# Optimization experiments

Measured on AMD Instinct MI355X. Metric: run time of the kernel, lower is better.

## Reference

```python
import jax, jax.numpy as jnp
import numpy as np

N, IN_DIM, HID, OUT, NH = 512, 256, 256, 256, 4
HD = OUT // NH  # head_dim = 64
EPS = 1e-5


def _mlp(x, w1, b1, w2, b2):
    return jax.nn.relu(x @ w1 + b1) @ w2 + b2


def setup_inputs() -> dict:
    key = jax.random.key(0)
    ks = jax.random.split(key, 32)

    def rn(k, shape, fan_in):
        return (jax.random.normal(k, shape, jnp.float32) / np.float32(np.sqrt(fan_in)))

    V = jax.random.normal(ks[0], (N, IN_DIM), jnp.float32)
    adj = jax.random.randint(ks[1], (N, N), 0, 2, jnp.int32)
    adj = adj.at[jnp.arange(N), jnp.arange(N)].set(1)  # self-edges: avoid all -inf rows
    prev_hidden = jax.random.normal(ks[2], (N, HID), jnp.float32)
    z = jnp.zeros
    return dict(
        V=V, adj=adj, prev_hidden=prev_hidden,
        W1=rn(ks[3], (IN_DIM, HID), IN_DIM),
        a_std0=rn(ks[4], (HID, 1), HID), a_std1=rn(ks[5], (HID, 1), HID),
        ce_w1=rn(ks[6], (2 * IN_DIM, HID), 2 * IN_DIM), ce_b1=z((HID,), jnp.float32),
        ce_w2=rn(ks[7], (HID, HD), HID), ce_b2=z((HD,), jnp.float32),
        a_c0=rn(ks[8], (HD, 1), HD), a_c1=rn(ks[9], (HD, 1), HD),
        te_w1=rn(ks[10], (IN_DIM + HID, HID), IN_DIM + HID), te_b1=z((HID,), jnp.float32),
        te_w2=rn(ks[11], (HID, HD), HID), te_b2=z((HD,), jnp.float32),
        a_t0=rn(ks[12], (HD, 1), HD), a_t1=rn(ks[13], (HD, 1), HD),
        co_w1=rn(ks[14], (3 * IN_DIM, HID), 3 * IN_DIM), co_b1=z((HID,), jnp.float32),
        co_w2=rn(ks[15], (HID, HD), HID), co_b2=z((HD,), jnp.float32),
        a_co0=rn(ks[16], (HD, 1), HD), a_co1=rn(ks[17], (HD, 1), HD),
        W2=rn(ks[18], (HID + 2 * HD + 1, OUT), HID + 2 * HD + 1),
        Wo=rn(ks[19], (OUT, OUT), OUT), bo=z((OUT,), jnp.float32),
        ln_g=jnp.ones((OUT,), jnp.float32), ln_b=z((OUT,), jnp.float32),
    )


def reference(V, adj, prev_hidden, W1, a_std0, a_std1,
              ce_w1, ce_b1, ce_w2, ce_b2, a_c0, a_c1,
              te_w1, te_b1, te_w2, te_b2, a_t0, a_t1,
              co_w1, co_b1, co_w2, co_b2, a_co0, a_co1,
              W2, Wo, bo, ln_g, ln_b):
    ninf = -jnp.inf

    # ---- standard GAT branch -> H1: (N, HID) ----
    Wh1 = V @ W1
    s1 = Wh1 @ a_std0 + (Wh1 @ a_std1).T                      # (N, N)
    s1 = jnp.where(adj == 0, ninf, s1)
    H1 = jax.nn.softmax(s1, axis=1) @ Wh1

    # ---- causal branch: all ordered pairs i!=j, global softmax -> H2: (N, HD) ----
    pair = jnp.concatenate([jnp.broadcast_to(V[:, None, :], (N, N, IN_DIM)),
                            jnp.broadcast_to(V[None, :, :], (N, N, IN_DIM))], axis=-1)
    cf = _mlp(pair, ce_w1, ce_b1, ce_w2, ce_b2)               # (N, N, HD)
    cs = (cf @ (a_c0 + a_c1))[..., 0]                         # (N, N)
    cs = jnp.where(jnp.eye(N, dtype=bool), ninf, cs)          # exclude i==j pairs
    ca = jax.nn.softmax(cs.reshape(-1)).reshape(N, N, 1)
    H2 = jnp.broadcast_to((ca * cf).sum((0, 1)), (N, HD))

    # ---- temporal branch: (N,1) scores broadcast against causal mask -> running mean ----
    tf = _mlp(jnp.concatenate([V, prev_hidden], axis=-1), te_w1, te_b1, te_w2, te_b2)  # (N, HD)
    ts = tf @ (a_t0 + a_t1)                                   # (N, 1)
    cmask = jnp.triu(jnp.ones((N, N), bool), 1)
    tsb = jnp.where(cmask, ninf, jnp.broadcast_to(ts, (N, N)))
    H3 = jax.nn.softmax(tsb, axis=1) @ tf                     # (N, HD)

    # ---- coop branch: first two neighbors by index; size-1 softmax; buggy pad -> (N,1) ----
    order = jnp.argsort((1 - adj).astype(jnp.int32), axis=1, stable=True)  # adj==1 first, index order
    nb = V[order[:, :2]]                                      # (N, 2, IN_DIM)
    valid = ((adj == 1).sum(axis=1) >= 2)
    nb = jnp.where(valid[:, None, None], nb, jnp.zeros_like(nb))
    ci = jnp.concatenate([V, nb[:, 0], nb[:, 1]], axis=-1)    # (N, 3*IN_DIM)
    cf4 = _mlp(ci, co_w1, co_b1, co_w2, co_b2)                # (N, HD)
    ca4 = jax.nn.softmax(cf4 @ (a_co0 + a_co1), axis=1)       # (N,1): softmax over size-1 -> ones
    h4vec = (ca4.T @ cf4)[0]                                  # (HD,)
    # original: squeeze(-2)->(HD,), dim==1 -> unsqueeze(-1)->(HD,1), zero-pad rows to N
    H4 = jnp.zeros((N, 1), V.dtype).at[:HD, 0].set(h4vec)

    # ---- combine, lazy W2, proj, LN, ELU (dropout identity in eval) ----
    Hc = jnp.concatenate([H1, H2, H3, H4], axis=-1) @ W2      # (N, OUT)
    out = Hc @ Wo + bo
    mu = out.mean(-1, keepdims=True)
    var = ((out - mu) ** 2).mean(-1, keepdims=True)
    out = (out - mu) / jnp.sqrt(var + EPS) * ln_g + ln_b
    return jax.nn.elu(out)
```

## Files before the change

### kernel.cpp

```cpp
#include <hip/hip_runtime.h>
#include <math.h>

#define NN 512
#define HD 64
#define EPSV 1e-5f

typedef unsigned short u16;
typedef short s4v __attribute__((ext_vector_type(4)));
typedef short s8v __attribute__((ext_vector_type(8)));
typedef float f4v __attribute__((ext_vector_type(4)));

struct GD {
  const float *A, *A2, *A3, *A4;
  const int* I;
  const float *B, *bias;
  float* C;
  const u16 *Bth, *Btl;
  u16 *Cth, *Ctl;
  int Bkp, Ckp;
  int M, K, Nn, mode, act;
};

#define GEMM_SMEM 28800
#define MEGA_SMEM 38656

__device__ __forceinline__ void split_bf16(float x, u16& h, u16& l) {
  unsigned xb = __float_as_uint(x);
  float hf = __uint_as_float(xb & 0xffff0000u);
  h = (u16)(xb >> 16);
  l = (u16)(__float_as_uint(x - hf) >> 16);
}

__device__ __forceinline__ void gemm_body(char* smem, const GD& d, int bx, int by) {
  u16 (*Ah)[72] = (u16(*)[72])smem;
  u16 (*Al)[72] = (u16(*)[72])(smem + 4608);
  u16 (*Bh)[68] = (u16(*)[68])(smem + 9216);
  u16 (*Bl)[68] = (u16(*)[68])(smem + 9216 + 8704);
  char* extra = smem + 26624;
  int* nbl = (int*)extra;
  float* wscl = (float*)extra;
  float* rowsuml = wscl + 512;

  const int t = threadIdx.x;
  const int rowbase = by * 32, colbase = bx * 64;
  const int K = d.K, Nn = d.Nn, mode = d.mode, M = d.M;
  if (rowbase >= M) return;

  if (mode == 2) {
    int wave = t >> 6, lane = t & 63;
    for (int rr = wave; rr < 32; rr += 4) {
      int row = rowbase + rr;
      int n0 = -1, n1 = -1, cnt = 0;
      for (int c = 0; c < 8; ++c) {
        unsigned long long mm = __ballot(d.I[row * NN + c * 64 + lane] != 0);
        cnt += (int)__popcll(mm);
        if (n0 < 0 && mm) { n0 = c * 64 + (int)__builtin_ctzll(mm); mm &= mm - 1; }
        if (n1 < 0 && mm) { n1 = c * 64 + (int)__builtin_ctzll(mm); }
      }
      if (lane == 0) { nbl[rr * 3] = n0; nbl[rr * 3 + 1] = n1; nbl[rr * 3 + 2] = (cnt >= 2); }
    }
    __syncthreads();
  } else if (mode == 4) {
    wscl[t] = d.A2[t];
    wscl[256 + t] = d.A2[256 + t];
    __syncthreads();
  }

  float4 aR[2], bR[4];
  s8v bp[4];
  float rs0 = 0.f, rs1 = 0.f;

  auto loadA = [&](int k0) {
#pragma unroll
    for (int j = 0; j < 2; ++j) {
      int idx = t + j * 256;
      int r = idx >> 4, c0 = (idx & 15) * 4;
      int row = rowbase + r, gk = k0 + c0;
      float4 v4 = make_float4(0.f, 0.f, 0.f, 0.f);
      if (mode == 0) {
        if (row < M && gk < K) v4 = *(const float4*)&d.A[(size_t)row * K + gk];
      } else if (mode == 1) {
        if (gk < 256) v4 = *(const float4*)&d.A[row * 256 + gk];
        else v4 = *(const float4*)&d.A2[row * 256 + gk - 256];
      } else if (mode == 2) {
        int seg = gk >> 8;
        int src = (seg == 0) ? row : (nbl[r * 3 + 2] ? nbl[r * 3 + seg - 1] : -1);
        if (src >= 0) v4 = *(const float4*)&d.A[src * 256 + (gk & 255)];
      } else if (mode == 3) {
        if (gk + 3 < 256) v4 = *(const float4*)&d.A[row * 256 + gk];
        else if (gk >= 256 && gk + 3 < 320) v4 = *(const float4*)&d.A2[gk - 256];
        else if (gk >= 320 && gk + 3 < 384) v4 = *(const float4*)&d.A3[row * 64 + gk - 320];
        else if (gk == 384) v4.x = (row < 64) ? d.A4[row] : 0.f;
      } else {
        int4 a4 = *(const int4*)&d.I[row * NN + gk];
        v4.x = a4.x ? wscl[gk + 0] : 0.f;
        v4.y = a4.y ? wscl[gk + 1] : 0.f;
        v4.z = a4.z ? wscl[gk + 2] : 0.f;
        v4.w = a4.w ? wscl[gk + 3] : 0.f;
        float ss = v4.x + v4.y + v4.z + v4.w;
        if (j == 0) rs0 += ss; else rs1 += ss;
      }
      aR[j] = v4;
    }
  };
  auto loadB = [&](int k0) {
    if (d.Bth) {
#pragma unroll
      for (int j = 0; j < 2; ++j) {
        int idx = t + j * 256;
        int n = idx >> 3, kb = (idx & 7) * 8;
        size_t base = (size_t)(colbase + n) * d.Bkp + k0 + kb;
        bp[j] = *(const s8v*)&d.Bth[base];
        bp[2 + j] = *(const s8v*)&d.Btl[base];
      }
    } else {
#pragma unroll
      for (int j = 0; j < 4; ++j) {
        int idx = t + j * 256;
        int r = idx >> 4, c0 = (idx & 15) * 4;
        int gk = k0 + r;
        float4 v4 = make_float4(0.f, 0.f, 0.f, 0.f);
        if (gk < K) v4 = *(const float4*)&d.B[(size_t)gk * Nn + colbase + c0];
        bR[j] = v4;
      }
    }
  };
  auto stos = [&]() {
#pragma unroll
    for (int j = 0; j < 2; ++j) {
      int idx = t + j * 256;
      int r = idx >> 4, c0 = (idx & 15) * 4;
      float v[4] = {aR[j].x, aR[j].y, aR[j].z, aR[j].w};
      u16 h[4], l[4];
#pragma unroll
      for (int e = 0; e < 4; ++e) split_bf16(v[e], h[e], l[e]);
      *(short4*)&Ah[r][c0] = make_short4((short)h[0], (short)h[1], (short)h[2], (short)h[3]);
      *(short4*)&Al[r][c0] = make_short4((short)l[0], (short)l[1], (short)l[2], (short)l[3]);
    }
    if (d.Bth) {
#pragma unroll
      for (int j = 0; j < 2; ++j) {
        int idx = t + j * 256;
        int n = idx >> 3, kb = (idx & 7) * 8;
        *(s8v*)&Bh[n][kb] = bp[j];
        *(s8v*)&Bl[n][kb] = bp[2 + j];
      }
    } else {
#pragma unroll
      for (int j = 0; j < 4; ++j) {
        int idx = t + j * 256;
        int r = idx >> 4, c0 = (idx & 15) * 4;
        float v[4] = {bR[j].x, bR[j].y, bR[j].z, bR[j].w};
#pragma unroll
        for (int e = 0; e < 4; ++e) {
          u16 h, l;
          split_bf16(v[e], h, l);
          Bh[c0 + e][r] = h;
          Bl[c0 + e][r] = l;
        }
      }
    }
  };

  f4v acc0 = {0.f, 0.f, 0.f, 0.f};
  f4v acc1 = {0.f, 0.f, 0.f, 0.f};

  const int w4 = t >> 6;
  const int lrow = t & 15;
  const int lk = ((t & 63) >> 4) * 8;

  int iters = (K + 63) >> 6;
  loadA(0); loadB(0);
  for (int it = 0; it < iters; ++it) {
    stos();
    __syncthreads();
    if (it + 1 < iters) { loadA((it + 1) << 6); loadB((it + 1) << 6); }
    const u16* bhrow = Bh[w4 * 16 + lrow];
    const u16* blrow = Bl[w4 * 16 + lrow];
#pragma unroll
    for (int ks = 0; ks < 2; ++ks) {
      int ko = ks * 32 + lk;
      s4v bh_0 = *(const s4v*)&bhrow[ko];
      s4v bh_1 = *(const s4v*)&bhrow[ko + 4];
      s4v bl_0 = *(const s4v*)&blrow[ko];
      s4v bl_1 = *(const s4v*)&blrow[ko + 4];
      s8v bh = __builtin_shufflevector(bh_0, bh_1, 0, 1, 2, 3, 4, 5, 6, 7);
      s8v bl = __builtin_shufflevector(bl_0, bl_1, 0, 1, 2, 3, 4, 5, 6, 7);
      {
        s8v ah = *(const s8v*)&Ah[lrow][ko];
        s8v al = *(const s8v*)&Al[lrow][ko];
        acc0 = __builtin_amdgcn_mfma_f32_16x16x32_bf16(ah, bh, acc0, 0, 0, 0);
        acc0 = __builtin_amdgcn_mfma_f32_16x16x32_bf16(ah, bl, acc0, 0, 0, 0);
        acc0 = __builtin_amdgcn_mfma_f32_16x16x32_bf16(al, bh, acc0, 0, 0, 0);
      }
      {
        s8v ah = *(const s8v*)&Ah[16 + lrow][ko];
        s8v al = *(const s8v*)&Al[16 + lrow][ko];
        acc1 = __builtin_amdgcn_mfma_f32_16x16x32_bf16(ah, bh, acc1, 0, 0, 0);
        acc1 = __builtin_amdgcn_mfma_f32_16x16x32_bf16(ah, bl, acc1, 0, 0, 0);
        acc1 = __builtin_amdgcn_mfma_f32_16x16x32_bf16(al, bh, acc1, 0, 0, 0);
      }
    }
    __syncthreads();
  }

  if (mode == 4) {
    float a0 = rs0, a1 = rs1;
#pragma unroll
    for (int off = 8; off; off >>= 1) {
      a0 += __shfl_xor(a0, off, 16);
      a1 += __shfl_xor(a1, off, 16);
    }
    if ((t & 15) == 0) { rowsuml[t >> 4] = a0; rowsuml[16 + (t >> 4)] = a1; }
    __syncthreads();
  }

  int col = colbase + w4 * 16 + lrow;
  int qrow = ((t & 63) >> 4) * 4;
  if (d.Cth) {
    size_t cb = (size_t)col * d.Ckp + rowbase + qrow;
#pragma unroll
    for (int m = 0; m < 2; ++m) {
      u16 hh[4], ll[4];
#pragma unroll
      for (int q = 0; q < 4; ++q) split_bf16(m ? acc1[q] : acc0[q], hh[q], ll[q]);
      *(short4*)&d.Cth[cb + m * 16] = make_short4((short)hh[0], (short)hh[1], (short)hh[2], (short)hh[3]);
      *(short4*)&d.Ctl[cb + m * 16] = make_short4((short)ll[0], (short)ll[1], (short)ll[2], (short)ll[3]);
    }
  }
  if (d.C) {
    float bvs = d.bias ? d.bias[col] : 0.f;
#pragma unroll
    for (int m = 0; m < 2; ++m) {
#pragma unroll
      for (int q = 0; q < 4; ++q) {
        int lr = m * 16 + qrow + q;
        int row = rowbase + lr;
        if (row >= M) continue;
        float o = (m ? acc1[q] : acc0[q]) + bvs;
        if (d.act) o = fmaxf(o, 0.f);
        if (mode == 4) o *= (1.f / rowsuml[lr]);
        d.C[(size_t)row * Nn + col] = o;
      }
    }
  }
}

__device__ void wsc_body(char* smem, const float* W1, const float* a_std1,
                         const float* V, float* expwsc, int grp) {
  float* asl = (float*)smem;
  float* ul  = asl + 256;
  int t = threadIdx.x;
  asl[t] = a_std1[t];
  __syncthreads();
  {
    float s = 0.f;
    const float* wr = W1 + t * 256;
    for (int h = 0; h < 256; h += 4) {
      float4 w4 = *(const float4*)&wr[h];
      float4 a4 = *(const float4*)&asl[h];
      s += w4.x * a4.x + w4.y * a4.y + w4.z * a4.z + w4.w * a4.w;
    }
    ul[t] = s;
  }
  __syncthreads();
  int wave = t >> 6, lane = t & 63;
  float4 u4 = *(const float4*)&ul[lane * 4];
  int j0 = grp * 128;
  for (int j = j0 + wave; j < j0 + 128; j += 4) {
    float4 v4 = *(const float4*)&V[j * 256 + lane * 4];
    float s = v4.x * u4.x + v4.y * u4.y + v4.z * u4.z + v4.w * u4.w;
#pragma unroll
    for (int off = 32; off; off >>= 1) s += __shfl_xor(s, off, 64);
    if (lane == 0) expwsc[j] = __expf(s);
  }
}

struct GD7 {
  GD d[7];
  const float *tw2, *cw2, *ce_w2, *a_c0, *a_c1;
  u16 *tw2h, *tw2l, *cw2h, *cw2l, *wfh, *wfl;
  float* wclg;
};

__device__ void conv_body(char* smem, int bx, const GD7& a) {
  float (*Ls)[66] = (float(*)[66])smem;
  int t = threadIdx.x;
  const float* src = (bx < 2) ? a.tw2 : a.cw2;
  u16* dh = (bx < 2) ? a.tw2h : a.cw2h;
  u16* dl = (bx < 2) ? a.tw2l : a.cw2l;
  int k0 = (bx & 1) * 128;
  for (int kt = 0; kt < 2; ++kt) {
    int k00 = k0 + kt * 64;
#pragma unroll
    for (int j = 0; j < 4; ++j) {
      int idx = t + j * 256;
      int r = idx >> 4, c = (idx & 15) * 4;
      *(float4*)&Ls[r][c] = *(const float4*)&src[(k00 + r) * 64 + c];
    }
    __syncthreads();
#pragma unroll
    for (int j = 0; j < 4; ++j) {
      int idx = t + j * 256;
      int n = idx >> 4, kk = (idx & 15) * 4;
      u16 hh[4], ll[4];
#pragma unroll
      for (int e = 0; e < 4; ++e) split_bf16(Ls[kk + e][n], hh[e], ll[e]);
      *(short4*)&dh[n * 256 + k00 + kk] = make_short4((short)hh[0], (short)hh[1], (short)hh[2], (short)hh[3]);
      *(short4*)&dl[n * 256 + k00 + kk] = make_short4((short)ll[0], (short)ll[1], (short)ll[2], (short)ll[3]);
    }
    __syncthreads();
  }
  if (bx == 3) {
    float s = 0.f;
    const float* w2r = a.ce_w2 + t * 64;
    for (int h = 0; h < 64; ++h) s += w2r[h] * (a.a_c0[h] + a.a_c1[h]);
    a.wclg[t] = s;
    int n = t;
    for (int kk = 416; kk < 448; kk += 4) {
      *(short4*)&a.wfh[n * 448 + kk] = make_short4(0, 0, 0, 0);
      *(short4*)&a.wfl[n * 448 + kk] = make_short4(0, 0, 0, 0);
    }
  }
}

__global__ __launch_bounds__(256) void gemm7_k(GD7 ds) {
  __shared__ __align__(16) char smem[GEMM_SMEM];
  int z = blockIdx.z;
  if (z == 6) {
    if (blockIdx.y == 0) { wsc_body(smem, ds.d[6].A, ds.d[6].A2, ds.d[6].A3, ds.d[6].C, blockIdx.x); return; }
    if (blockIdx.y == 1) { conv_body(smem, blockIdx.x, ds); return; }
    return;
  }
  gemm_body(smem, ds.d[z], blockIdx.x, blockIdx.y);
}
__global__ __launch_bounds__(256) void gemm1_k(GD d) {
  __shared__ __align__(16) char smem[GEMM_SMEM];
  gemm_body(smem, d, blockIdx.x, blockIdx.y);
}

__device__ void pair_body(char* smem,
    const float* __restrict__ P, const float* __restrict__ Q,
    const float* __restrict__ b1, const float* __restrict__ ce_w2,
    const float* __restrict__ wclg,
    float* __restrict__ mpart, float* __restrict__ dpart,
    float* __restrict__ spart, int byy, int bxx) {
  float* Pl  = (float*)smem;
  float* Ql  = Pl + 16 * 260;
  float* el  = Ql + 16 * 260;
  float* wcl = el + 16 * 20;
  float* red = wcl + 256;
  float* sk  = red + 256;
  float* sbl = sk + 256;
  int t = threadIdx.x;

  wcl[t] = wclg[t];
  int i0 = byy * 16, j0 = bxx * 16;
  for (int e = t; e < 1024; e += 256) {
    int r = e >> 6, c4 = (e & 63) * 4;
    float4 bb = *(const float4*)&b1[c4];
    float4 pv = *(const float4*)&P[(i0 + r) * 256 + c4];
    pv.x += bb.x; pv.y += bb.y; pv.z += bb.z; pv.w += bb.w;
    *(float4*)&Pl[r * 260 + c4] = pv;
    *(float4*)&Ql[r * 260 + c4] = *(const float4*)&Q[(j0 + r) * 256 + c4];
  }
  __syncthreads();

  int a = t >> 4, b = t & 15;
  const float* pr = &Pl[a * 260];
  const float* qr = &Ql[b * 260];
  float4 c4a = make_float4(0.f, 0.f, 0.f, 0.f);
#pragma unroll 8
  for (int k4 = 0; k4 < 64; ++k4) {
    float4 w = *(const float4*)&wcl[k4 * 4];
    float4 p = *(const float4*)&pr[k4 * 4];
    float4 q = *(const float4*)&qr[k4 * 4];
    c4a.x += fmaxf(p.x + q.x, 0.f) * w.x;
    c4a.y += fmaxf(p.y + q.y, 0.f) * w.y;
    c4a.z += fmaxf(p.z + q.z, 0.f) * w.z;
    c4a.w += fmaxf(p.w + q.w, 0.f) * w.w;
  }
  float s = c4a.x + c4a.y + c4a.z + c4a.w;
  if (i0 + a == j0 + b) s = -INFINITY;
  float wm = s;
#pragma unroll
  for (int off = 32; off; off >>= 1) wm = fmaxf(wm, __shfl_xor(wm, off, 64));
  if ((t & 63) == 0) red[t >> 6] = wm;
  __syncthreads();
  float mb = fmaxf(fmaxf(red[0], red[1]), fmaxf(red[2], red[3]));
  float e = __expf(s - mb);
  el[a * 20 + b] = e;
  float ws2 = e;
#pragma unroll
  for (int off = 32; off; off >>= 1) ws2 += __shfl_xor(ws2, off, 64);
  if ((t & 63) == 0) red[8 + (t >> 6)] = ws2;
  __syncthreads();
  float db = red[8] + red[9] + red[10] + red[11];

  float qv[16];
#pragma unroll
  for (int j = 0; j < 16; ++j) qv[j] = Ql[j * 260 + t];
  float rk = 0.f;
#pragma unroll 4
  for (int i = 0; i < 16; ++i) {
    float pv = Pl[i * 260 + t];
    const float* erow = &el[i * 20];
#pragma unroll
    for (int j4 = 0; j4 < 4; ++j4) {
      float4 e4 = *(const float4*)&erow[j4 * 4];
      rk += e4.x * fmaxf(pv + qv[j4 * 4 + 0], 0.f);
      rk += e4.y * fmaxf(pv + qv[j4 * 4 + 1], 0.f);
      rk += e4.z * fmaxf(pv + qv[j4 * 4 + 2], 0.f);
      rk += e4.w * fmaxf(pv + qv[j4 * 4 + 3], 0.f);
    }
  }
  sk[t] = rk;
  __syncthreads();
  {
    int h = t & 63, q = t >> 6;
    float s2 = 0.f;
    for (int k = q * 64; k < q * 64 + 64; ++k) s2 += sk[k] * ce_w2[k * 64 + h];
    sbl[q * 64 + h] = s2;
  }
  __syncthreads();
  int blk = byy * 32 + bxx;
  if (t < 64) spart[blk * 64 + t] = sbl[t] + sbl[64 + t] + sbl[128 + t] + sbl[192 + t];
  if (t == 0) { mpart[blk] = mb; dpart[blk] = db; }
}

struct MegaArgs {
  const float *P, *Q, *b1, *ce_w2, *wclg;
  float *mpart, *dpart, *spart;
  GD gH1, gTf, gCf;
};

__global__ __launch_bounds__(256) void mega_k(MegaArgs a) {
  __shared__ __align__(16) char smem[MEGA_SMEM];
  int b = blockIdx.x;
  if (b < 64) {
    gemm_body(smem, a.gH1, b & 3, b >> 2);
  } else if (b < 80) {
    gemm_body(smem, a.gTf, 0, b - 64);
  } else if (b < 96) {
    gemm_body(smem, a.gCf, 0, b - 80);
  } else {
    int p = b - 96;
    pair_body(smem, a.P, a.Q, a.b1, a.ce_w2, a.wclg,
              a.mpart, a.dpart, a.spart, p >> 5, p & 31);
  }
}

__global__ __launch_bounds__(1024) void mini_k(
    const float* __restrict__ mpart, const float* __restrict__ dpart,
    const float* __restrict__ spart, const float* __restrict__ ce_b2,
    float* __restrict__ H2row,
    const float* __restrict__ tf, float* __restrict__ H3,
    const float* __restrict__ cf4, float* __restrict__ h4vec) {
  __shared__ float A[1024];
  __shared__ float Bsh[1024];
  __shared__ float segsum[16][65];
  int b = blockIdx.x, t = threadIdx.x;
  if (b == 0) {
    float mv = mpart[t];
    A[t] = mv; __syncthreads();
    for (int s = 512; s; s >>= 1) { if (t < s) A[t] = fmaxf(A[t], A[t + s]); __syncthreads(); }
    float M = A[0];
    __syncthreads();
    float e = __expf(mv - M);
    Bsh[t] = e;
    A[t] = e * dpart[t];
    __syncthreads();
    for (int s = 512; s; s >>= 1) { if (t < s) A[t] += A[t + s]; __syncthreads(); }
    float D = A[0];
    __syncthreads();
    int h = t & 63, g = t >> 6;
    float s2 = 0.f;
    for (int b2 = g * 64; b2 < g * 64 + 64; ++b2) s2 += Bsh[b2] * spart[b2 * 64 + h];
    A[t] = s2;
    __syncthreads();
    for (int p = 8; p; p >>= 1) { if (g < p) A[g * 64 + h] += A[(g + p) * 64 + h]; __syncthreads(); }
    if (t < 64) H2row[t] = A[t] / D + ce_b2[t];
  } else if (b == 1) {
    int h = t & 63, g = t >> 6;
    float vals[32];
    float run = 0.f;
#pragma unroll
    for (int r = 0; r < 32; ++r) { run += tf[(g * 32 + r) * 64 + h]; vals[r] = run; }
    segsum[g][h] = run;
    __syncthreads();
    float off = 0.f;
    for (int gg = 0; gg < g; ++gg) off += segsum[gg][h];
#pragma unroll
    for (int r = 0; r < 32; ++r) {
      int i = g * 32 + r;
      H3[i * 64 + h] = (vals[r] + off) / (float)(i + 1);
    }
  } else {
    int h = t & 63, g = t >> 6;
    float s = 0.f;
    for (int r = 0; r < 32; ++r) s += cf4[(g * 32 + r) * 64 + h];
    A[g * 64 + h] = s;
    __syncthreads();
    for (int p = 8; p; p >>= 1) { if (g < p) A[g * 64 + h] += A[(g + p) * 64 + h]; __syncthreads(); }
    if (t < 64) h4vec[t] = A[t];
  }
}

__global__ void ln_elu_kernel(const float* __restrict__ X, const float* __restrict__ g,
                              const float* __restrict__ b, float* __restrict__ out) {
  __shared__ float red[256];
  int i = blockIdx.x, tid = threadIdx.x;
  float x = X[i * 256 + tid];
  red[tid] = x; __syncthreads();
  for (int s = 128; s; s >>= 1) { if (tid < s) red[tid] += red[tid + s]; __syncthreads(); }
  float mu = red[0] * (1.f / 256.f);
  __syncthreads();
  float d = x - mu;
  red[tid] = d * d; __syncthreads();
  for (int s = 128; s; s >>= 1) { if (tid < s) red[tid] += red[tid + s]; __syncthreads(); }
  float var = red[0] * (1.f / 256.f);
  float y = d / sqrtf(var + EPSV) * g[tid] + b[tid];
  out[i * 256 + tid] = (y > 0.f) ? y : (expf(y) - 1.f);
}

static GD mkgd(const float* A, const float* A2, const float* A3, const float* A4,
               const int* I, const float* B, const float* bias, float* C,
               int M, int K, int Nn, int mode, int act) {
  GD g{A, A2, A3, A4, I, B, bias, C, 0, 0, 0, 0, 0, 0, M, K, Nn, mode, act};
  return g;
}

extern "C" void kernel_launch(void* const* d_in, const int* in_sizes, int n_in,
                              void* d_out, int out_size, void* d_ws, size_t ws_size,
                              hipStream_t stream) {
  const float* V      = (const float*)d_in[0];
  const int*   adj    = (const int*)  d_in[1];
  const float* ph     = (const float*)d_in[2];
  const float* W1     = (const float*)d_in[3];
  const float* a_std1 = (const float*)d_in[5];
  const float* ce_w1  = (const float*)d_in[6];
  const float* ce_b1  = (const float*)d_in[7];
  const float* ce_w2  = (const float*)d_in[8];
  const float* ce_b2  = (const float*)d_in[9];
  const float* a_c0   = (const float*)d_in[10];
  const float* a_c1   = (const float*)d_in[11];
  const float* te_w1  = (const float*)d_in[12];
  const float* te_b1  = (const float*)d_in[13];
  const float* te_w2  = (const float*)d_in[14];
  const float* te_b2  = (const float*)d_in[15];
  const float* co_w1  = (const float*)d_in[18];
  const float* co_b1  = (const float*)d_in[19];
  const float* co_w2  = (const float*)d_in[20];
  const float* co_b2  = (const float*)d_in[21];
  const float* W2     = (const float*)d_in[24];
  const float* Wo     = (const float*)d_in[25];
  const float* bo     = (const float*)d_in[26];
  const float* ln_g   = (const float*)d_in[27];
  const float* ln_b   = (const float*)d_in[28];
  float* out = (float*)d_out;

  float* ws = (float*)d_ws;
  size_t off = 0;
  auto alloc = [&](size_t n) { float* p = ws + off; off += (n + 15) & ~(size_t)15; return p; };

  float* Pb     = alloc(512 * 256);
  float* Qb     = alloc(512 * 256);
  float* tfh    = alloc(512 * 256);
  float* cf4h   = alloc(512 * 256);
  float* H1     = alloc(512 * 256);
  float* T2     = alloc(512 * 256);
  float* tf     = alloc(512 * 64);
  float* cf4    = alloc(512 * 64);
  float* H3     = alloc(512 * 64);
  float* spart  = alloc(1024 * 64);
  float* mpart  = alloc(1024);
  float* dpart  = alloc(1024);
  float* expwsc = alloc(512);
  float* H2row  = alloc(64);
  float* h4vec  = alloc(64);
  u16* Wh1t_h = (u16*)alloc(65536);
  u16* Wh1t_l = (u16*)alloc(65536);
  u16* Wf_h   = (u16*)alloc(57344);
  u16* Wf_l   = (u16*)alloc(57344);
  u16* tw2h   = (u16*)alloc(8192);
  u16* tw2l   = (u16*)alloc(8192);
  u16* cw2h   = (u16*)alloc(8192);
  u16* cw2l   = (u16*)alloc(8192);
  float* wclg = alloc(256);
  (void)ws_size; (void)in_sizes; (void)n_in; (void)out_size;

  GD7 sA;
  sA.d[0] = mkgd(V, 0, 0, 0, 0, W1, 0, 0, 512, 256, 256, 0, 0);
  sA.d[0].Cth = Wh1t_h; sA.d[0].Ctl = Wh1t_l; sA.d[0].Ckp = 512;
  sA.d[1] = mkgd(V, 0, 0, 0, 0, ce_w1, 0, Pb, 512, 256, 256, 0, 0);
  sA.d[2] = mkgd(V, 0, 0, 0, 0, ce_w1 + 256 * 256, 0, Qb, 512, 256, 256, 0, 0);
  sA.d[3] = mkgd(V, ph, 0, 0, 0, te_w1, te_b1, tfh, 512, 512, 256, 1, 1);
  sA.d[4] = mkgd(V, 0, 0, 0, adj, co_w1, co_b1, cf4h, 512, 768, 256, 2, 1);
  sA.d[5] = mkgd(W2, 0, 0, 0, 0, Wo, 0, 0, 385, 256, 256, 0, 0);
  sA.d[5].Cth = Wf_h; sA.d[5].Ctl = Wf_l; sA.d[5].Ckp = 448;
  sA.d[6] = mkgd(W1, a_std1, V, 0, 0, 0, 0, expwsc, 512, 256, 1, 6, 0);
  sA.tw2 = te_w2; sA.cw2 = co_w2; sA.ce_w2 = ce_w2; sA.a_c0 = a_c0; sA.a_c1 = a_c1;
  sA.tw2h = tw2h; sA.tw2l = tw2l; sA.cw2h = cw2h; sA.cw2l = cw2l;
  sA.wfh = Wf_h; sA.wfl = Wf_l; sA.wclg = wclg;
  gemm7_k<<<dim3(4, 16, 7), 256, 0, stream>>>(sA);

  MegaArgs ma;
  ma.P = Pb; ma.Q = Qb; ma.b1 = ce_b1; ma.ce_w2 = ce_w2; ma.wclg = wclg;
  ma.mpart = mpart; ma.dpart = dpart; ma.spart = spart;
  ma.gH1 = mkgd(0, expwsc, 0, 0, adj, 0, 0, H1, 512, 512, 256, 4, 0);
  ma.gH1.Bth = Wh1t_h; ma.gH1.Btl = Wh1t_l; ma.gH1.Bkp = 512;
  ma.gTf = mkgd(tfh, 0, 0, 0, 0, 0, te_b2, tf, 512, 256, 64, 0, 0);
  ma.gTf.Bth = tw2h; ma.gTf.Btl = tw2l; ma.gTf.Bkp = 256;
  ma.gCf = mkgd(cf4h, 0, 0, 0, 0, 0, co_b2, cf4, 512, 256, 64, 0, 0);
  ma.gCf.Bth = cw2h; ma.gCf.Btl = cw2l; ma.gCf.Bkp = 256;
  mega_k<<<1120, 256, 0, stream>>>(ma);

  mini_k<<<3, 1024, 0, stream>>>(mpart, dpart, spart, ce_b2, H2row, tf, H3, cf4, h4vec);

  GD gF = mkgd(H1, H2row, H3, h4vec, 0, 0, bo, T2, 512, 385, 256, 3, 0);
  gF.Bth = Wf_h; gF.Btl = Wf_l; gF.Bkp = 448;
  gemm1_k<<<dim3(4, 16), 256, 0, stream>>>(gF);

  ln_elu_kernel<<<512, 256, 0, stream>>>(T2, ln_g, ln_b, out);
}
```

Measured before the change: 191.2 us.

## Fuse final GEMM with LayerNorm+ELU via last-block counter; trim mega grid

Removes the separate LayerNorm/ELU launch. The last of the four column blocks to finish a 32-row stripe of the final GEMM, detected with an atomic counter reset in the first kernel, normalizes those rows using wave-level shuffle reductions. Separately, the mega kernel grid shrinks from 1120 to 1024 blocks, and the first 96 pair blocks each process a second pair tile to cover the dropped blocks. This saves one launch and an extra pass over the intermediate, but it relies on threadfence/atomic ordering and lengthens the tail of some pair blocks.

```diff
diff --git a/kernel.cpp b/kernel.cpp
--- a/kernel.cpp
+++ b/kernel.cpp
@@ -281,6 +281,7 @@
   const float *tw2, *cw2, *ce_w2, *a_c0, *a_c1;
   u16 *tw2h, *tw2l, *cw2h, *cw2l, *wfh, *wfl;
   float* wclg;
+  unsigned* cnts;
 };
 
 __device__ void conv_body(char* smem, int bx, const GD7& a) {
@@ -312,6 +313,7 @@
     __syncthreads();
   }
   if (bx == 3) {
+    if (t < 16) a.cnts[t] = 0u;
     float s = 0.f;
     const float* w2r = a.ce_w2 + t * 64;
     for (int h = 0; h < 64; ++h) s += w2r[h] * (a.a_c0[h] + a.a_c1[h]);
@@ -333,10 +335,6 @@
     return;
   }
   gemm_body(smem, ds.d[z], blockIdx.x, blockIdx.y);
-}
-__global__ __launch_bounds__(256) void gemm1_k(GD d) {
-  __shared__ __align__(16) char smem[GEMM_SMEM];
-  gemm_body(smem, d, blockIdx.x, blockIdx.y);
 }
 
 __device__ void pair_body(char* smem,
@@ -447,6 +445,12 @@
     int p = b - 96;
     pair_body(smem, a.P, a.Q, a.b1, a.ce_w2, a.wclg,
               a.mpart, a.dpart, a.spart, p >> 5, p & 31);
+    if (p < 96) {
+      int p2 = 928 + p;
+      __syncthreads();
+      pair_body(smem, a.P, a.Q, a.b1, a.ce_w2, a.wclg,
+                a.mpart, a.dpart, a.spart, p2 >> 5, p2 & 31);
+    }
   }
 }
 
@@ -506,21 +510,46 @@
   }
 }
 
-__global__ void ln_elu_kernel(const float* __restrict__ X, const float* __restrict__ g,
-                              const float* __restrict__ b, float* __restrict__ out) {
-  __shared__ float red[256];
-  int i = blockIdx.x, tid = threadIdx.x;
-  float x = X[i * 256 + tid];
-  red[tid] = x; __syncthreads();
-  for (int s = 128; s; s >>= 1) { if (tid < s) red[tid] += red[tid + s]; __syncthreads(); }
-  float mu = red[0] * (1.f / 256.f);
-  __syncthreads();
-  float d = x - mu;
-  red[tid] = d * d; __syncthreads();
-  for (int s = 128; s; s >>= 1) { if (tid < s) red[tid] += red[tid + s]; __syncthreads(); }
-  float var = red[0] * (1.f / 256.f);
-  float y = d / sqrtf(var + EPSV) * g[tid] + b[tid];
-  out[i * 256 + tid] = (y > 0.f) ? y : (expf(y) - 1.f);
+__global__ __launch_bounds__(256) void gemm_ln_k(GD d, const float* __restrict__ lng,
+                                                 const float* __restrict__ lnb,
+                                                 float* __restrict__ out, unsigned* cnts) {
+  __shared__ __align__(16) char smem[GEMM_SMEM];
+  gemm_body(smem, d, blockIdx.x, blockIdx.y);
+  __syncthreads();
+  __threadfence();
+  __shared__ unsigned po;
+  if (threadIdx.x == 0) po = atomicAdd(&cnts[blockIdx.y], 1u);
+  __syncthreads();
+  if (po == 3u) {
+    __threadfence();
+    int t = threadIdx.x, lane = t & 63, w = t >> 6;
+    const float* T2 = d.C;
+    for (int r8 = 0; r8 < 8; ++r8) {
+      int row = blockIdx.y * 32 + w * 8 + r8;
+      float4 x = *(const float4*)&T2[row * 256 + lane * 4];
+      float s = x.x + x.y + x.z + x.w;
+#pragma unroll
+      for (int off = 32; off; off >>= 1) s += __shfl_xor(s, off, 64);
+      float mu = s * (1.f / 256.f);
+      float4 dv = make_float4(x.x - mu, x.y - mu, x.z - mu, x.w - mu);
+      float s2 = dv.x * dv.x + dv.y * dv.y + dv.z * dv.z + dv.w * dv.w;
+#pragma unroll
+      for (int off = 32; off; off >>= 1) s2 += __shfl_xor(s2, off, 64);
+      float rstd = 1.f / sqrtf(s2 * (1.f / 256.f) + EPSV);
+      float4 gg = *(const float4*)&lng[lane * 4];
+      float4 bb = *(const float4*)&lnb[lane * 4];
+      float4 y;
+      y.x = dv.x * rstd * gg.x + bb.x;
+      y.y = dv.y * rstd * gg.y + bb.y;
+      y.z = dv.z * rstd * gg.z + bb.z;
+      y.w = dv.w * rstd * gg.w + bb.w;
+      y.x = (y.x > 0.f) ? y.x : (expf(y.x) - 1.f);
+      y.y = (y.y > 0.f) ? y.y : (expf(y.y) - 1.f);
+      y.z = (y.z > 0.f) ? y.z : (expf(y.z) - 1.f);
+      y.w = (y.w > 0.f) ? y.w : (expf(y.w) - 1.f);
+      *(float4*)&out[row * 256 + lane * 4] = y;
+    }
+  }
 }
 
 static GD mkgd(const float* A, const float* A2, const float* A3, const float* A4,
@@ -587,6 +616,7 @@
   u16* cw2h   = (u16*)alloc(8192);
   u16* cw2l   = (u16*)alloc(8192);
   float* wclg = alloc(256);
+  unsigned* cnts = (unsigned*)alloc(64);
   (void)ws_size; (void)in_sizes; (void)n_in; (void)out_size;
 
   GD7 sA;
@@ -601,7 +631,7 @@
   sA.d[6] = mkgd(W1, a_std1, V, 0, 0, 0, 0, expwsc, 512, 256, 1, 6, 0);
   sA.tw2 = te_w2; sA.cw2 = co_w2; sA.ce_w2 = ce_w2; sA.a_c0 = a_c0; sA.a_c1 = a_c1;
   sA.tw2h = tw2h; sA.tw2l = tw2l; sA.cw2h = cw2h; sA.cw2l = cw2l;
-  sA.wfh = Wf_h; sA.wfl = Wf_l; sA.wclg = wclg;
+  sA.wfh = Wf_h; sA.wfl = Wf_l; sA.wclg = wclg; sA.cnts = cnts;
   gemm7_k<<<dim3(4, 16, 7), 256, 0, stream>>>(sA);
 
   MegaArgs ma;
@@ -613,13 +643,11 @@
   ma.gTf.Bth = tw2h; ma.gTf.Btl = tw2l; ma.gTf.Bkp = 256;
   ma.gCf = mkgd(cf4h, 0, 0, 0, 0, 0, co_b2, cf4, 512, 256, 64, 0, 0);
   ma.gCf.Bth = cw2h; ma.gCf.Btl = cw2l; ma.gCf.Bkp = 256;
-  mega_k<<<1120, 256, 0, stream>>>(ma);
+  mega_k<<<1024, 256, 0, stream>>>(ma);
 
   mini_k<<<3, 1024, 0, stream>>>(mpart, dpart, spart, ce_b2, H2row, tf, H3, cf4, h4vec);
 
   GD gF = mkgd(H1, H2row, H3, h4vec, 0, 0, bo, T2, 512, 385, 256, 3, 0);
   gF.Bth = Wf_h; gF.Btl = Wf_l; gF.Bkp = 448;
-  gemm1_k<<<dim3(4, 16), 256, 0, stream>>>(gF);
-
-  ln_elu_kernel<<<512, 256, 0, stream>>>(T2, ln_g, ln_b, out);
-}
+  gemm_ln_k<<<dim3(4, 16), 256, 0, stream>>>(gF, ln_g, ln_b, out, cnts);
+}
```

Result: slower. 214.4 us (+12.2%).
